# Optimization experiments

Measured on AMD Instinct MI355X. Metric: run time of the kernel, lower is better.

The kernel has to match this reference:

```python
import jax, jax.numpy as jnp
import numpy as np

# Config (matches init_kwargs + Mamba2 defaults: expand=2, headdim=64, ngroups=1)
B_, C_IN, T, H, W = 4, 23, 8, 128, 128
P = 4
DM = 256
D_STATE = 16
D_CONV = 4
EXPAND = 2
D_INNER = EXPAND * DM            # 512
HEADDIM = 64
NHEADS = D_INNER // HEADDIM      # 8
CONV_DIM = D_INNER + 2 * D_STATE # 544 (ngroups=1)
D_IN_PROJ = 2 * D_INNER + 2 * D_STATE + NHEADS


def setup_inputs() -> dict:
    key = jax.random.key(0)
    ks = jax.random.split(key, 12)
    s = lambda k, shape, sc: (jax.random.normal(k, shape, jnp.float32) * sc)
    x = jax.random.normal(ks[0], (B_, C_IN, T, H, W), jnp.float32)
    patch_w = s(ks[1], (DM, C_IN, P, P), 0.05)       # Conv3d weight, depth-1 dim squeezed
    patch_b = s(ks[2], (DM,), 0.02)
    W_in = s(ks[3], (DM, D_IN_PROJ), 0.05)           # in_proj (bias=False)
    conv_w = s(ks[4], (CONV_DIM, D_CONV), 0.2)       # depthwise conv1d weight
    conv_b = s(ks[5], (CONV_DIM,), 0.02)
    dt_bias = jnp.log(jnp.expm1(jnp.exp(jax.random.uniform(ks[6], (NHEADS,), jnp.float32, jnp.log(1e-3), jnp.log(1e-1)))))
    A_log = jnp.log(jnp.arange(1, NHEADS + 1, dtype=jnp.float32))
    D_param = jnp.ones((NHEADS,), jnp.float32)
    norm_w = jnp.ones((D_INNER,), jnp.float32)
    W_out = s(ks[7], (D_INNER, DM), 0.05)            # out_proj (bias=False)
    unembed_w = s(ks[8], (DM, C_IN, P, P), 0.05)     # ConvTranspose3d weight (in,out,1,p,p)
    unembed_b = s(ks[9], (C_IN,), 0.02)
    return {"x": x, "patch_w": patch_w, "patch_b": patch_b, "W_in": W_in,
            "conv_w": conv_w, "conv_b": conv_b, "dt_bias": dt_bias, "A_log": A_log,
            "D_param": D_param, "norm_w": norm_w, "W_out": W_out,
            "unembed_w": unembed_w, "unembed_b": unembed_b}


def reference(x, patch_w, patch_b, W_in, conv_w, conv_b, dt_bias, A_log,
              D_param, norm_w, W_out, unembed_w, unembed_b):
    B, C, Tt, Hh, Ww = x.shape
    p = patch_w.shape[-1]
    Hp, Wp = Hh // p, Ww // p
    L = Tt * Hp * Wp
    # --- Conv3d patch embed (kernel (1,p,p), stride (1,p,p)) == non-overlapping patchify ---
    xr = x.reshape(B, C, Tt, Hp, p, Wp, p)
    emb = jnp.einsum('bcthiwj,dcij->bthwd', xr, patch_w) + patch_b  # [B,T,Hp,Wp,D]
    xs = emb.reshape(B, L, DM)
    # --- Mamba2 ---
    zxbcdt = xs @ W_in                                 # [B,L,2*d_inner+2*d_state+nheads]
    z = zxbcdt[:, :, :D_INNER]
    xBC = zxbcdt[:, :, D_INNER:D_INNER + CONV_DIM]
    dt = zxbcdt[:, :, D_INNER + CONV_DIM:]             # [B,L,nheads]
    # causal depthwise conv1d + silu
    xp = jnp.pad(xBC, ((0, 0), (D_CONV - 1, 0), (0, 0)))
    conv_out = conv_b + sum(xp[:, k:k + L, :] * conv_w[:, k] for k in range(D_CONV))
    xBC = jax.nn.silu(conv_out)
    xh = xBC[:, :, :D_INNER].reshape(B, L, NHEADS, HEADDIM)
    Bm = xBC[:, :, D_INNER:D_INNER + D_STATE]          # [B,L,N] (ngroups=1)
    Cm = xBC[:, :, D_INNER + D_STATE:]                 # [B,L,N]
    dt = jax.nn.softplus(dt + dt_bias)                 # [B,L,H]
    A = -jnp.exp(A_log)                                # [H]
    dA = jnp.exp(dt * A)                               # [B,L,H]
    xdt = xh * dt[..., None]                           # [B,L,H,P]
    # selective state-space scan: h_t = dA_t h_{t-1} + (dt_t x_t) B_t^T ; y_t = h_t C_t
    def step(h, inp):
        dA_t, xdt_t, B_t, C_t = inp
        h = dA_t[..., None, None] * h + jnp.einsum('bhp,bn->bhpn', xdt_t, B_t)
        y = jnp.einsum('bhpn,bn->bhp', h, C_t)
        return h, y
    inps = (dA.transpose(1, 0, 2), xdt.transpose(1, 0, 2, 3),
            Bm.transpose(1, 0, 2), Cm.transpose(1, 0, 2))
    h0 = jnp.zeros((B, NHEADS, HEADDIM, D_STATE), xs.dtype)
    _, ys = jax.lax.scan(step, h0, inps)               # [L,B,H,P]
    y = ys.transpose(1, 0, 2, 3) + D_param[None, None, :, None] * xh
    y = y.reshape(B, L, D_INNER)
    # gated RMSNorm (norm_before_gate=False): rmsnorm(y * silu(z)) * w
    yg = y * jax.nn.silu(z)
    y = yg * jax.lax.rsqrt(jnp.mean(yg * yg, axis=-1, keepdims=True) + 1e-5) * norm_w
    out_seq = y @ W_out                                # [B,L,DM]
    # --- ConvTranspose3d unembed (kernel (1,p,p), stride (1,p,p)) == un-patchify ---
    outp = out_seq.reshape(B, Tt, Hp, Wp, DM)
    un = jnp.einsum('bthwd,dcij->bcthiwj', outp, unembed_w)
    out = un.reshape(B, C, Tt, Hh, Ww) + unembed_b[None, :, None, None, None]
    return out + x
```

## Files before the change

### kernel.cpp

```cpp
#include <hip/hip_runtime.h>
#include <hip/hip_bf16.h>
#include <cstdint>
#include <cstddef>

#define B_N       4
#define C_INCH    23
#define T_N       8
#define W_IMG     128
#define L_SEQ     8192
#define BLROWS    32768
#define DM_       256
#define D_INNER_  512
#define CONV_DIM_ 544
#define D_PROJ    1064
#define KPATCH    368
#define QCH       64
#define NCH       128
#define RECW      56

typedef unsigned short ushort_t;
typedef unsigned int uint_t;
typedef __attribute__((ext_vector_type(8))) short short8;
typedef __attribute__((ext_vector_type(4))) float f32x4;

__device__ __forceinline__ float b2f(ushort_t u) {
    union { float f; uint_t u; } v; v.u = ((uint_t)u) << 16; return v.f;
}
__device__ __forceinline__ ushort_t f2b(float f) {
    union { float f; uint_t u; } v; v.f = f;
    uint_t r = v.u + 0x7fffu + ((v.u >> 16) & 1u);
    return (ushort_t)(r >> 16);
}

__device__ __forceinline__ void gload_lds16(const ushort_t* g, ushort_t* l) {
    __builtin_amdgcn_global_load_lds(
        (const __attribute__((address_space(1))) unsigned int*)g,
        (__attribute__((address_space(3))) unsigned int*)l, 16, 0, 0);
}

__device__ __forceinline__ short8 frag8(const float* q, bool live) {
    short8 f;
    if (live) {
        float4 lo = *(const float4*)q, hi = *(const float4*)(q + 4);
        f[0] = (short)f2b(lo.x); f[1] = (short)f2b(lo.y);
        f[2] = (short)f2b(lo.z); f[3] = (short)f2b(lo.w);
        f[4] = (short)f2b(hi.x); f[5] = (short)f2b(hi.y);
        f[6] = (short)f2b(hi.z); f[7] = (short)f2b(hi.w);
    } else {
        #pragma unroll
        for (int e = 0; e < 8; ++e) f[e] = 0;
    }
    return f;
}

__device__ __forceinline__ uint_t gate2(uint_t yw, uint_t zw) {
    float y0 = b2f((ushort_t)(yw & 0xffffu)), y1 = b2f((ushort_t)(yw >> 16));
    float z0 = b2f((ushort_t)(zw & 0xffffu)), z1 = b2f((ushort_t)(zw >> 16));
    return (uint_t)f2b(y0 * z0) | ((uint_t)f2b(y1 * z1) << 16);
}

__global__ void k_transcast(const float* __restrict__ src, ushort_t* __restrict__ dst,
                            int K, int N, const float* __restrict__ rscale) {
    int n = blockIdx.x;
    for (int k = threadIdx.x; k < K; k += 256) {
        float v = 0.f;
        if (n < N) {
            v = src[(size_t)k * N + n];
            if (rscale) v *= rscale[k];
        }
        dst[(size_t)n * K + k] = f2b(v);
    }
}

__global__ void k_castpad(const float* __restrict__ src, ushort_t* __restrict__ dst) {
    int d = blockIdx.x; int k = threadIdx.x;
    dst[d * 384 + k] = (k < KPATCH) ? f2b(src[d * KPATCH + k]) : (ushort_t)0;
}

__global__ void __launch_bounds__(256) k_pgemm(const float* __restrict__ x,
                                               const ushort_t* __restrict__ Wt,
                                               ushort_t* __restrict__ Cv,
                                               const float* __restrict__ bias) {
    __shared__ ushort_t Al[128 * 64];
    __shared__ ushort_t Bl[128 * 64];
    const int tid = threadIdx.x;
    const int w = tid >> 6, lane = tid & 63;
    const int wr = w >> 1, wc = w & 1;
    const int rowbase = blockIdx.y * 128;
    const int colbase = blockIdx.x * 128;
    const int g = lane >> 4, r = lane & 15;
    const int b  = rowbase >> 13;
    const int t  = (rowbase >> 10) & 7;
    const int hp0 = (rowbase >> 5) & 31;

    f32x4 acc[4][4];
    #pragma unroll
    for (int i = 0; i < 4; ++i)
        #pragma unroll
        for (int j = 0; j < 4; ++j) acc[i][j] = (f32x4){0.f, 0.f, 0.f, 0.f};

    for (int it = 0; it < 6; ++it) {
        int k0 = it * 64;
        __syncthreads();
        #pragma unroll
        for (int i2 = 0; i2 < 4; ++i2) {
            int s = i2 * 256 + (w << 6) + lane;
            int row = s >> 3;
            int c16 = (s & 7) ^ (row & 7);
            gload_lds16(Wt + (size_t)(colbase + row) * 384 + k0 + c16 * 8,
                        &Bl[(size_t)(i2 * 256 + (w << 6)) * 8]);
        }
        #pragma unroll
        for (int i2 = 0; i2 < 8; ++i2) {
            int idx = i2 * 256 + tid;
            int row = idx >> 4, kq = idx & 15;
            int c = (k0 >> 4) + (kq >> 2);
            int i = kq & 3;
            uint_t u0 = 0, u1 = 0;
            if (c < C_INCH) {
                int hp = hp0 + (row >> 5), wp = row & 31;
                const float4 v = *(const float4*)&x[(((size_t)(b * C_INCH + c) * T_N + t) << 14)
                                                    + (size_t)(hp * 4 + i) * W_IMG + wp * 4];
                u0 = (uint_t)f2b(v.x) | ((uint_t)f2b(v.y) << 16);
                u1 = (uint_t)f2b(v.z) | ((uint_t)f2b(v.w) << 16);
            }
            int slot = (row << 3) + ((kq >> 1) ^ (row & 7));
            *(uint2*)&Al[(size_t)slot * 8 + (kq & 1) * 4] = make_uint2(u0, u1);
        }
        __syncthreads();

        short8 af[2][4], bf[2][4];
        #pragma unroll
        for (int ks = 0; ks < 2; ++ks)
            #pragma unroll
            for (int mi = 0; mi < 4; ++mi) {
                int row = (wr << 6) + (mi << 4) + r;
                int c16 = ((ks << 2) | g) ^ (row & 7);
                af[ks][mi] = *(const short8*)&Al[(size_t)((row << 3) + c16) * 8];
            }
        #pragma unroll
        for (int ks = 0; ks < 2; ++ks)
            #pragma unroll
            for (int ni = 0; ni < 4; ++ni) {
                int row = (wc << 6) + (ni << 4) + r;
                int c16 = ((ks << 2) | g) ^ (row & 7);
                bf[ks][ni] = *(const short8*)&Bl[(size_t)((row << 3) + c16) * 8];
            }
        #pragma unroll
        for (int ks = 0; ks < 2; ++ks)
            #pragma unroll
            for (int mi = 0; mi < 4; ++mi)
                #pragma unroll
                for (int ni = 0; ni < 4; ++ni)
                    acc[mi][ni] = __builtin_amdgcn_mfma_f32_16x16x32_bf16(
                        af[ks][mi], bf[ks][ni], acc[mi][ni], 0, 0, 0);
    }

    #pragma unroll
    for (int mi = 0; mi < 4; ++mi) {
        int rw = rowbase + (wr << 6) + (mi << 4) + (g << 2);
        #pragma unroll
        for (int ni = 0; ni < 4; ++ni) {
            int col = colbase + (wc << 6) + (ni << 4) + r;
            float bv = bias[col];
            f32x4 v = acc[mi][ni];
            #pragma unroll
            for (int j = 0; j < 4; ++j)
                Cv[(size_t)(rw + j) * DM_ + col] = f2b(v[j] + bv);
        }
    }
}

template <int K, int N, bool CBF, bool ASCALE, bool SILU>
__global__ void __launch_bounds__(256) k_mgemm(const ushort_t* __restrict__ A, const int lda,
                                               const ushort_t* __restrict__ Wt,
                                               void* __restrict__ Cv, const int ldc, const int coff,
                                               const float* __restrict__ bias) {
    __shared__ ushort_t Al[128 * 64];
    __shared__ ushort_t Bl[128 * 64];
    const int tid = threadIdx.x;
    const int w = tid >> 6, lane = tid & 63;
    const int wr = w >> 1, wc = w & 1;
    const int rowbase = blockIdx.y * 128;
    const int colbase = blockIdx.x * 128;
    const int g = lane >> 4, r = lane & 15;

    f32x4 acc[4][4];
    #pragma unroll
    for (int i = 0; i < 4; ++i)
        #pragma unroll
        for (int j = 0; j < 4; ++j) acc[i][j] = (f32x4){0.f, 0.f, 0.f, 0.f};
    float rs[4] = {0.f, 0.f, 0.f, 0.f};

    for (int k0 = 0; k0 < K; k0 += 64) {
        __syncthreads();
        #pragma unroll
        for (int it = 0; it < 4; ++it) {
            int s = it * 256 + (w << 6) + lane;
            int row = s >> 3;
            int c16 = (s & 7) ^ (row & 7);
            gload_lds16(A + (size_t)(rowbase + row) * lda + k0 + c16 * 8,
                        &Al[(size_t)(it * 256 + (w << 6)) * 8]);
        }
        #pragma unroll
        for (int it = 0; it < 4; ++it) {
            int s = it * 256 + (w << 6) + lane;
            int row = s >> 3;
            int c16 = (s & 7) ^ (row & 7);
            gload_lds16(Wt + (size_t)(colbase + row) * K + k0 + c16 * 8,
                        &Bl[(size_t)(it * 256 + (w << 6)) * 8]);
        }
        __syncthreads();

        short8 af[2][4], bf[2][4];
        #pragma unroll
        for (int ks = 0; ks < 2; ++ks)
            #pragma unroll
            for (int mi = 0; mi < 4; ++mi) {
                int row = (wr << 6) + (mi << 4) + r;
                int c16 = ((ks << 2) | g) ^ (row & 7);
                af[ks][mi] = *(const short8*)&Al[(size_t)((row << 3) + c16) * 8];
            }
        #pragma unroll
        for (int ks = 0; ks < 2; ++ks)
            #pragma unroll
            for (int ni = 0; ni < 4; ++ni) {
                int row = (wc << 6) + (ni << 4) + r;
                int c16 = ((ks << 2) | g) ^ (row & 7);
                bf[ks][ni] = *(const short8*)&Bl[(size_t)((row << 3) + c16) * 8];
            }
        if (ASCALE) {
            #pragma unroll
            for (int ks = 0; ks < 2; ++ks)
                #pragma unroll
                for (int mi = 0; mi < 4; ++mi)
                    #pragma unroll
                    for (int e = 0; e < 8; ++e) {
                        float v = b2f((ushort_t)af[ks][mi][e]);
                        rs[mi] += v * v;
                    }
        }
        #pragma unroll
        for (int ks = 0; ks < 2; ++ks)
            #pragma unroll
            for (int mi = 0; mi < 4; ++mi)
                #pragma unroll
                for (int ni = 0; ni < 4; ++ni)
                    acc[mi][ni] = __builtin_amdgcn_mfma_f32_16x16x32_bf16(
                        af[ks][mi], bf[ks][ni], acc[mi][ni], 0, 0, 0);
    }

    #pragma unroll
    for (int mi = 0; mi < 4; ++mi) {
        int rw = rowbase + (wr << 6) + (mi << 4) + (g << 2);
        float sj[4] = {1.f, 1.f, 1.f, 1.f};
        if (ASCALE) {
            float s = rs[mi];
            s += __shfl_xor(s, 16);
            s += __shfl_xor(s, 32);
            float sc = rsqrtf(s * (1.f / 512.f) + 1e-5f);
            #pragma unroll
            for (int j = 0; j < 4; ++j) sj[j] = __shfl(sc, 4 * g + j);
        }
        #pragma unroll
        for (int ni = 0; ni < 4; ++ni) {
            int col = colbase + (wc << 6) + (ni << 4) + r;
            if (col < N) {
                float bv = bias ? bias[col] : 0.f;
                f32x4 v = acc[mi][ni];
                #pragma unroll
                for (int j = 0; j < 4; ++j) {
                    size_t cidx = (size_t)(rw + j) * ldc + coff + col;
                    float vr = v[j] * sj[j] + bv;
                    if (SILU) vr = vr / (1.f + __expf(-vr));
                    if (CBF) ((ushort_t*)Cv)[cidx] = f2b(vr);
                    else     ((float*)Cv)[cidx]   = vr;
                }
            }
        }
    }
}

__global__ void __launch_bounds__(256) k_conv(const ushort_t* __restrict__ xbcdt,
                                              const float* __restrict__ cw,
                                              const float* __restrict__ cb,
                                              const float* __restrict__ dtb,
                                              const float* __restrict__ alog,
                                              ushort_t* __restrict__ xbc,
                                              float* __restrict__ brec) {
    int tid = threadIdx.x;
    int rb = blockIdx.x * 8;
    int srb = rb & (L_SEQ - 1);
    #pragma unroll
    for (int it = 0; it < 3; ++it) {
        int ch = it * 256 + tid;
        if (ch >= 552) break;
        if (ch < CONV_DIM_) {
            float w0 = cw[ch * 4 + 0], w1 = cw[ch * 4 + 1];
            float w2 = cw[ch * 4 + 2], w3 = cw[ch * 4 + 3];
            float bias = cb[ch];
            float win[11];
            #pragma unroll
            for (int j = 0; j < 11; ++j) {
                int sj = srb + j - 3;
                win[j] = (sj >= 0) ? b2f(xbcdt[(size_t)(rb + j - 3) * 640 + ch]) : 0.f;
            }
            #pragma unroll
            for (int r = 0; r < 8; ++r) {
                float acc = bias + win[r] * w0 + win[r + 1] * w1 + win[r + 2] * w2 + win[r + 3] * w3;
                float s = acc / (1.f + __expf(-acc));
                size_t row = rb + r;
                if (ch < 512) xbc[row * 512 + ch] = f2b(s);
                else          brec[row * RECW + (ch - 512)] = s;
            }
        } else {
            int h = ch - CONV_DIM_;
            float A = -__expf(alog[h]);
            float db = dtb[h];
            #pragma unroll
            for (int r = 0; r < 8; ++r) {
                size_t row = rb + r;
                float v = b2f(xbcdt[row * 640 + ch]) + db;
                float sp = (v > 20.f) ? v : log1pf(__expf(v));
                brec[row * RECW + 32 + h] = __expf(sp * A);
                brec[row * RECW + 40 + h] = sp;
                brec[row * RECW + 48 + h] = sp * A;
            }
        }
    }
}

__device__ __forceinline__ void stage_xht(const ushort_t* __restrict__ xbc,
                                          size_t row0, int h, int tid,
                                          ushort_t* __restrict__ XhT) {
    int j = tid & 63, q4 = tid >> 6;
    const uint4* xsrc = (const uint4*)(xbc + (row0 + j) * 512 + h * 64);
    uint4 xa = xsrc[q4 * 2], xb = xsrc[q4 * 2 + 1];
    #pragma unroll
    for (int pp = 0; pp < 16; ++pp) {
        int p = q4 * 16 + pp;
        uint4 v = (pp < 8) ? xa : xb;
        int sub = (pp >> 1) & 3;
        uint_t word = (sub == 0) ? v.x : (sub == 1) ? v.y : (sub == 2) ? v.z : v.w;
        XhT[p * 72 + j] = (ushort_t)((pp & 1) ? (word >> 16) : (word & 0xffffu));
    }
}

__global__ void __launch_bounds__(256) k_scan1m(const ushort_t* __restrict__ xbc,
                                                const float* __restrict__ brec,
                                                float* __restrict__ sbuf,
                                                float* __restrict__ cdf) {
    __shared__ ushort_t XhT[64 * 72];
    __shared__ float    Bst[64 * 20];
    __shared__ ushort_t BwT[16 * 72];
    const int c = blockIdx.x, h = blockIdx.y, b = blockIdx.z;
    const int tid = threadIdx.x;
    const int w = tid >> 6, lane = tid & 63;
    const int g = lane >> 4, r = lane & 15;
    const size_t row0 = (size_t)b * L_SEQ + (size_t)c * QCH;

    {
        int row = tid >> 2, q = tid & 3;
        float4 v = *(const float4*)(brec + (row0 + row) * RECW + q * 4);
        *(float4*)&Bst[row * 20 + q * 4] = v;
    }
    stage_xht(xbc, row0, h, tid, XhT);

    if (w == 0) {
        float ldA = brec[(row0 + lane) * RECW + 48 + h];
        float dtv = brec[(row0 + lane) * RECW + 40 + h];
        float S = ldA;
        #pragma unroll
        for (int d = 1; d < 64; d <<= 1) {
            float o = __shfl(S, (lane >= d) ? (lane - d) : 0);
            if (lane >= d) S += o;
        }
        float Stot = __shfl(S, 63);
        float wj = dtv * __expf(Stot - S);
        __builtin_amdgcn_s_barrier();
        const float* bp = &Bst[lane * 20];
        float4 b0 = *(const float4*)bp;
        float4 b1 = *(const float4*)(bp + 4);
        float4 b2 = *(const float4*)(bp + 8);
        float4 b3 = *(const float4*)(bp + 12);
        float bv[16] = {b0.x,b0.y,b0.z,b0.w, b1.x,b1.y,b1.z,b1.w,
                        b2.x,b2.y,b2.z,b2.w, b3.x,b3.y,b3.z,b3.w};
        #pragma unroll
        for (int n = 0; n < 16; ++n)
            BwT[n * 72 + lane] = f2b(bv[n] * wj);
        if (lane == 63) cdf[(b * 8 + h) * NCH + c] = __expf(S);
    } else {
        __builtin_amdgcn_s_barrier();
    }
    __syncthreads();

    short8 bwtf[2];
    bwtf[0] = *(const short8*)&BwT[r * 72 + 0  + g * 8];
    bwtf[1] = *(const short8*)&BwT[r * 72 + 32 + g * 8];

    size_t base = ((size_t)(b * 8 + h) * NCH + c) * 1024;
    {
        int p0t = w;
        short8 a0 = *(const short8*)&XhT[(p0t * 16 + r) * 72 + 0  + g * 8];
        short8 a1 = *(const short8*)&XhT[(p0t * 16 + r) * 72 + 32 + g * 8];
        f32x4 acc = (f32x4){0.f, 0.f, 0.f, 0.f};
        acc = __builtin_amdgcn_mfma_f32_16x16x32_bf16(a0, bwtf[0], acc, 0, 0, 0);
        acc = __builtin_amdgcn_mfma_f32_16x16x32_bf16(a1, bwtf[1], acc, 0, 0, 0);
        #pragma unroll
        for (int reg = 0; reg < 4; ++reg)
            sbuf[base + (size_t)(p0t * 16 + g * 4 + reg) * 16 + r] = acc[reg];
    }
}

__global__ void __launch_bounds__(256) k_chain(const float* __restrict__ sbuf,
                                               const float* __restrict__ cdf,
                                               float* __restrict__ hin) {
    int h = blockIdx.x, b = blockIdx.y;
    int tid = threadIdx.x;
    float4 H = make_float4(0.f, 0.f, 0.f, 0.f);
    size_t base = (size_t)((b * 8 + h) * NCH) * 1024;
    for (int c = 0; c < NCH; ++c) {
        *(float4*)&hin[base + (size_t)c * 1024 + tid * 4] = H;
        float cdfv = cdf[(b * 8 + h) * NCH + c];
        float4 S = *(const float4*)&sbuf[base + (size_t)c * 1024 + tid * 4];
        H.x = cdfv * H.x + S.x;
        H.y = cdfv * H.y + S.y;
        H.z = cdfv * H.z + S.z;
        H.w = cdfv * H.w + S.w;
    }
}

__global__ void __launch_bounds__(256) k_ssc2(const ushort_t* __restrict__ xbc,
                                              const ushort_t* __restrict__ z_bf,
                                              const float* __restrict__ brec,
                                              const float* __restrict__ Dp,
                                              const float* __restrict__ hin,
                                              ushort_t* __restrict__ yg_out) {
    __shared__ ushort_t XhT[64 * 72];
    __shared__ ushort_t Pl [64 * 72];
    __shared__ float Sl[64], Tl[64], El[64];
    const int c = blockIdx.x, h = blockIdx.y, b = blockIdx.z;
    const int tid = threadIdx.x;
    const int w = tid >> 6, lane = tid & 63;
    const int g = lane >> 4, r = lane & 15;
    const size_t row0 = (size_t)b * L_SEQ + (size_t)c * QCH;
    const size_t bhc = (size_t)(b * 8 + h) * NCH + c;

    #pragma unroll
    for (int it2 = 0; it2 < 2; ++it2) {
        int idx = it2 * 256 + tid;
        int row = idx >> 3, q = idx & 7;
        float4 v = *(const float4*)(brec + (row0 + row) * RECW + q * 4);
        uint_t u0 = (uint_t)f2b(v.x) | ((uint_t)f2b(v.y) << 16);
        uint_t u1 = (uint_t)f2b(v.z) | ((uint_t)f2b(v.w) << 16);
        *(uint2*)&Pl[row * 40 + q * 4] = make_uint2(u0, u1);
    }
    stage_xht(xbc, row0, h, tid, XhT);

    if (w == 0) {
        float ldA = brec[(row0 + lane) * RECW + 48 + h];
        float dtv = brec[(row0 + lane) * RECW + 40 + h];
        float S = ldA;
        #pragma unroll
        for (int d = 1; d < 64; d <<= 1) {
            float o = __shfl(S, (lane >= d) ? (lane - d) : 0);
            if (lane >= d) S += o;
        }
        Sl[lane] = S;
        Tl[lane] = S - __logf(dtv);
        El[lane] = __expf(S);
    }
    __syncthreads();

    short8 cwf, bwf[4];
    #pragma unroll
    for (int t4 = 0; t4 < 4; ++t4) {
        if (g < 2) {
            bwf[t4] = *(const short8*)&Pl[(t4 * 16 + r) * 40 + 0 + g * 8];
        } else {
            #pragma unroll
            for (int e = 0; e < 8; ++e) bwf[t4][e] = 0;
        }
    }
    if (g < 2) {
        cwf = *(const short8*)&Pl[(w * 16 + r) * 40 + 16 + g * 8];
    } else {
        #pragma unroll
        for (int e = 0; e < 8; ++e) cwf[e] = 0;
    }
    __syncthreads();

    {
        int i = w * 16 + r;
        float si = Sl[i];
        #pragma unroll
        for (int j0t = 0; j0t < 4; ++j0t) {
            f32x4 m = (f32x4){0.f, 0.f, 0.f, 0.f};
            m = __builtin_amdgcn_mfma_f32_16x16x32_bf16(bwf[j0t], cwf, m, 0, 0, 0);
            float4 tj = *(const float4*)&Tl[j0t * 16 + g * 4];
            ushort_t pv[4];
            #pragma unroll
            for (int reg = 0; reg < 4; ++reg) {
                int j = j0t * 16 + g * 4 + reg;
                float tjv = (reg == 0) ? tj.x : (reg == 1) ? tj.y : (reg == 2) ? tj.z : tj.w;
                float mask = (j <= i) ? __expf(si - tjv) : 0.f;
                pv[reg] = f2b(m[reg] * mask);
            }
            uint2 packed = make_uint2((uint_t)pv[0] | ((uint_t)pv[1] << 16),
                                      (uint_t)pv[2] | ((uint_t)pv[3] << 16));
            *(uint2*)&Pl[i * 72 + j0t * 16 + g * 4] = packed;
        }
    }
    __syncthreads();

    short8 pa0 = *(const short8*)&Pl[(w * 16 + r) * 72 + 0  + g * 8];
    short8 pa1 = *(const short8*)&Pl[(w * 16 + r) * 72 + 32 + g * 8];
    short8 xhf[4][2];
    #pragma unroll
    for (int p0t = 0; p0t < 4; ++p0t)
        #pragma unroll
        for (int kk = 0; kk < 2; ++kk)
            xhf[p0t][kk] = *(const short8*)&XhT[(p0t * 16 + r) * 72 + kk * 32 + g * 8];
    short8 hinf[4];
    #pragma unroll
    for (int p0t = 0; p0t < 4; ++p0t)
        hinf[p0t] = frag8(hin + bhc * 1024 + (size_t)(p0t * 16 + r) * 16 + g * 8, g < 2);

    const float Dh = Dp[h];
    float4 e4 = *(const float4*)&El[w * 16 + g * 4];
    __syncthreads();

    #pragma unroll
    for (int p0t = 0; p0t < 4; ++p0t) {
        f32x4 acc = (f32x4){0.f, 0.f, 0.f, 0.f};
        acc = __builtin_amdgcn_mfma_f32_16x16x32_bf16(cwf, hinf[p0t], acc, 0, 0, 0);
        acc[0] *= e4.x; acc[1] *= e4.y; acc[2] *= e4.z; acc[3] *= e4.w;
        acc = __builtin_amdgcn_mfma_f32_16x16x32_bf16(pa0, xhf[p0t][0], acc, 0, 0, 0);
        acc = __builtin_amdgcn_mfma_f32_16x16x32_bf16(pa1, xhf[p0t][1], acc, 0, 0, 0);
        int p = p0t * 16 + r;
        #pragma unroll
        for (int reg = 0; reg < 4; ++reg) {
            int i = w * 16 + g * 4 + reg;
            float xhv = b2f(XhT[p * 72 + i]);
            Pl[i * 72 + p] = f2b(acc[reg] + Dh * xhv);
        }
    }
    __syncthreads();

    #pragma unroll
    for (int it6 = 0; it6 < 2; ++it6) {
        int t = it6 * 256 + tid;
        int i = t >> 3, seg = t & 7;
        size_t row = row0 + i;
        uint4 yv = *(const uint4*)&Pl[i * 72 + seg * 8];
        uint4 zv = *(const uint4*)(z_bf + row * 512 + h * 64 + seg * 8);
        uint4 ov;
        ov.x = gate2(yv.x, zv.x);
        ov.y = gate2(yv.y, zv.y);
        ov.z = gate2(yv.z, zv.z);
        ov.w = gate2(yv.w, zv.w);
        *(uint4*)(yg_out + row * 512 + h * 64 + seg * 8) = ov;
    }
}

__global__ void __launch_bounds__(256) k_scatter(const ushort_t* __restrict__ tmp,
                                                 const float* __restrict__ ub,
                                                 const float* __restrict__ xin,
                                                 float* __restrict__ out) {
    int tid = threadIdx.x;
    int w = tid & 127;
    int h = (blockIdx.x << 1) | (tid >> 7);
    int c = blockIdx.y >> 3, t = blockIdx.y & 7;
    int b = blockIdx.z;
    size_t row = (size_t)b * L_SEQ + t * 1024 + (h >> 2) * 32 + (w >> 2);
    int kk = c * 16 + (h & 3) * 4 + (w & 3);
    size_t oidx = (((size_t)(b * C_INCH + c) * T_N + t) << 14) + (size_t)h * W_IMG + w;
    out[oidx] = b2f(tmp[row * KPATCH + kk]) + ub[c] + xin[oidx];
}

extern "C" void kernel_launch(void* const* d_in, const int* in_sizes, int n_in,
                              void* d_out, int out_size, void* d_ws, size_t ws_size,
                              hipStream_t stream) {
    const float* x       = (const float*)d_in[0];
    const float* patch_w = (const float*)d_in[1];
    const float* patch_b = (const float*)d_in[2];
    const float* W_in    = (const float*)d_in[3];
    const float* conv_w  = (const float*)d_in[4];
    const float* conv_b  = (const float*)d_in[5];
    const float* dt_bias = (const float*)d_in[6];
    const float* A_log   = (const float*)d_in[7];
    const float* D_param = (const float*)d_in[8];
    const float* norm_w  = (const float*)d_in[9];
    const float* W_out   = (const float*)d_in[10];
    const float* unemb_w = (const float*)d_in[11];
    const float* unemb_b = (const float*)d_in[12];
    float* out = (float*)d_out;

    char* p = (char*)d_ws;
    ushort_t* scratch = (ushort_t*)p; p += (size_t)BLROWS * 384 * 2;
    float* cdf  = (float*)p;   p += (size_t)32 * NCH * 4;
    float* sbuf = (float*)p;   p += (size_t)32 * NCH * 1024 * 4;
    float* hin  = (float*)p;   p += (size_t)32 * NCH * 1024 * 4;
    float* brec = (float*)p;   p += (size_t)BLROWS * RECW * 4;
    ushort_t* Wt_p   = (ushort_t*)p; p += (size_t)256 * 384 * 2;
    ushort_t* Wt_in  = (ushort_t*)p; p += (size_t)1152 * 256 * 2;
    ushort_t* Wt_out = (ushort_t*)p; p += (size_t)256 * 512 * 2;
    ushort_t* Wt_un  = (ushort_t*)p; p += (size_t)384 * 256 * 2;
    ushort_t* xs     = (ushort_t*)p; p += (size_t)BLROWS * DM_ * 2;
    ushort_t* xbc    = (ushort_t*)p; p += (size_t)BLROWS * 512 * 2;
    ushort_t* z_bf   = (ushort_t*)p; p += (size_t)BLROWS * 512 * 2;
    ushort_t* xbcdt  = (ushort_t*)p; p += (size_t)BLROWS * 640 * 2;
    size_t need = (size_t)(p - (char*)d_ws);
    if (ws_size < need) return;

    ushort_t* tmp = scratch;
    ushort_t* yg  = xbcdt;

    k_castpad<<<256, 384, 0, stream>>>(patch_w, Wt_p);
    k_transcast<<<1152, 256, 0, stream>>>(W_in, Wt_in, 256, 1064, nullptr);
    k_transcast<<<256, 256, 0, stream>>>(W_out, Wt_out, 512, 256, norm_w);
    k_transcast<<<384, 256, 0, stream>>>(unemb_w, Wt_un, 256, 368, nullptr);

    k_pgemm<<<dim3(2, 256), 256, 0, stream>>>(x, Wt_p, xs, patch_b);

    k_mgemm<256, 512, true, false, true><<<dim3(4, 256), 256, 0, stream>>>(xs, 256, Wt_in, z_bf, 512, 0, nullptr);
    k_mgemm<256, 552, true, false, false><<<dim3(5, 256), 256, 0, stream>>>(xs, 256, Wt_in + (size_t)512 * 256, xbcdt, 640, 0, nullptr);

    k_conv<<<BLROWS / 8, 256, 0, stream>>>(xbcdt, conv_w, conv_b, dt_bias, A_log, xbc, brec);

    k_scan1m<<<dim3(NCH, 8, 4), 256, 0, stream>>>(xbc, brec, sbuf, cdf);
    k_chain<<<dim3(8, 4), 256, 0, stream>>>(sbuf, cdf, hin);
    k_ssc2<<<dim3(NCH, 8, 4), 256, 0, stream>>>(xbc, z_bf, brec, D_param, hin, yg);

    k_mgemm<512, 256, true, true, false><<<dim3(2, 256), 256, 0, stream>>>(yg, 512, Wt_out, xs, DM_, 0, nullptr);

    k_mgemm<256, 368, true, false, false><<<dim3(3, 256), 256, 0, stream>>>(xs, 256, Wt_un, tmp, KPATCH, 0, nullptr);

    k_scatter<<<dim3(64, 184, 4), 256, 0, stream>>>(tmp, unemb_b, x, out);
}
```

Baseline: 243.4 us.

## Fold out_proj and unembed weights into one combined GEMM; unroll chain loop

```diff
diff --git a/kernel.cpp b/kernel.cpp
--- a/kernel.cpp
+++ b/kernel.cpp
@@ -60,14 +60,10 @@
 }
 
 __global__ void k_transcast(const float* __restrict__ src, ushort_t* __restrict__ dst,
-                            int K, int N, const float* __restrict__ rscale) {
+                            int K, int N) {
     int n = blockIdx.x;
     for (int k = threadIdx.x; k < K; k += 256) {
-        float v = 0.f;
-        if (n < N) {
-            v = src[(size_t)k * N + n];
-            if (rscale) v *= rscale[k];
-        }
+        float v = (n < N) ? src[(size_t)k * N + n] : 0.f;
         dst[(size_t)n * K + k] = f2b(v);
     }
 }
@@ -75,6 +71,33 @@
 __global__ void k_castpad(const float* __restrict__ src, ushort_t* __restrict__ dst) {
     int d = blockIdx.x; int k = threadIdx.x;
     dst[d * 384 + k] = (k < KPATCH) ? f2b(src[d * KPATCH + k]) : (ushort_t)0;
+}
+
+__global__ void __launch_bounds__(256) k_wcomb(const float* __restrict__ W_out,
+                                               const float* __restrict__ W_un,
+                                               const float* __restrict__ nw,
+                                               ushort_t* __restrict__ Wt) {
+    int n = blockIdx.x;
+    int tid = threadIdx.x;
+    #pragma unroll
+    for (int half = 0; half < 2; ++half) {
+        int mp = half * 256 + tid;
+        float acc = 0.f;
+        if (n < KPATCH) {
+            const float4* wo4 = (const float4*)(W_out + (size_t)mp * 256);
+            #pragma unroll 4
+            for (int d4 = 0; d4 < 64; ++d4) {
+                float4 wo = wo4[d4];
+                int d = d4 * 4;
+                acc += wo.x * W_un[(size_t)(d + 0) * KPATCH + n]
+                     + wo.y * W_un[(size_t)(d + 1) * KPATCH + n]
+                     + wo.z * W_un[(size_t)(d + 2) * KPATCH + n]
+                     + wo.w * W_un[(size_t)(d + 3) * KPATCH + n];
+            }
+            acc *= nw[mp];
+        }
+        Wt[(size_t)n * 512 + mp] = f2b(acc);
+    }
 }
 
 __global__ void __launch_bounds__(256) k_pgemm(const float* __restrict__ x,
@@ -419,14 +442,23 @@
     int tid = threadIdx.x;
     float4 H = make_float4(0.f, 0.f, 0.f, 0.f);
     size_t base = (size_t)((b * 8 + h) * NCH) * 1024;
-    for (int c = 0; c < NCH; ++c) {
-        *(float4*)&hin[base + (size_t)c * 1024 + tid * 4] = H;
-        float cdfv = cdf[(b * 8 + h) * NCH + c];
-        float4 S = *(const float4*)&sbuf[base + (size_t)c * 1024 + tid * 4];
-        H.x = cdfv * H.x + S.x;
-        H.y = cdfv * H.y + S.y;
-        H.z = cdfv * H.z + S.z;
-        H.w = cdfv * H.w + S.w;
+    const float* cdp = cdf + (size_t)(b * 8 + h) * NCH;
+    for (int c0 = 0; c0 < NCH; c0 += 4) {
+        float4 S[4];
+        float cd[4];
+        #pragma unroll
+        for (int j = 0; j < 4; ++j) {
+            S[j]  = *(const float4*)&sbuf[base + (size_t)(c0 + j) * 1024 + tid * 4];
+            cd[j] = cdp[c0 + j];
+        }
+        #pragma unroll
+        for (int j = 0; j < 4; ++j) {
+            *(float4*)&hin[base + (size_t)(c0 + j) * 1024 + tid * 4] = H;
+            H.x = cd[j] * H.x + S[j].x;
+            H.y = cd[j] * H.y + S[j].y;
+            H.z = cd[j] * H.z + S[j].z;
+            H.w = cd[j] * H.w + S[j].w;
+        }
     }
 }
 
@@ -602,10 +634,9 @@
     float* sbuf = (float*)p;   p += (size_t)32 * NCH * 1024 * 4;
     float* hin  = (float*)p;   p += (size_t)32 * NCH * 1024 * 4;
     float* brec = (float*)p;   p += (size_t)BLROWS * RECW * 4;
-    ushort_t* Wt_p   = (ushort_t*)p; p += (size_t)256 * 384 * 2;
-    ushort_t* Wt_in  = (ushort_t*)p; p += (size_t)1152 * 256 * 2;
-    ushort_t* Wt_out = (ushort_t*)p; p += (size_t)256 * 512 * 2;
-    ushort_t* Wt_un  = (ushort_t*)p; p += (size_t)384 * 256 * 2;
+    ushort_t* Wt_p    = (ushort_t*)p; p += (size_t)256 * 384 * 2;
+    ushort_t* Wt_in   = (ushort_t*)p; p += (size_t)1152 * 256 * 2;
+    ushort_t* Wt_comb = (ushort_t*)p; p += (size_t)384 * 512 * 2;
     ushort_t* xs     = (ushort_t*)p; p += (size_t)BLROWS * DM_ * 2;
     ushort_t* xbc    = (ushort_t*)p; p += (size_t)BLROWS * 512 * 2;
     ushort_t* z_bf   = (ushort_t*)p; p += (size_t)BLROWS * 512 * 2;
@@ -617,9 +648,8 @@
     ushort_t* yg  = xbcdt;
 
     k_castpad<<<256, 384, 0, stream>>>(patch_w, Wt_p);
-    k_transcast<<<1152, 256, 0, stream>>>(W_in, Wt_in, 256, 1064, nullptr);
-    k_transcast<<<256, 256, 0, stream>>>(W_out, Wt_out, 512, 256, norm_w);
-    k_transcast<<<384, 256, 0, stream>>>(unemb_w, Wt_un, 256, 368, nullptr);
+    k_transcast<<<1152, 256, 0, stream>>>(W_in, Wt_in, 256, 1064);
+    k_wcomb<<<384, 256, 0, stream>>>(W_out, unemb_w, norm_w, Wt_comb);
 
     k_pgemm<<<dim3(2, 256), 256, 0, stream>>>(x, Wt_p, xs, patch_b);
 
@@ -632,9 +662,7 @@
     k_chain<<<dim3(8, 4), 256, 0, stream>>>(sbuf, cdf, hin);
     k_ssc2<<<dim3(NCH, 8, 4), 256, 0, stream>>>(xbc, z_bf, brec, D_param, hin, yg);
 
-    k_mgemm<512, 256, true, true, false><<<dim3(2, 256), 256, 0, stream>>>(yg, 512, Wt_out, xs, DM_, 0, nullptr);
-
-    k_mgemm<256, 368, true, false, false><<<dim3(3, 256), 256, 0, stream>>>(xs, 256, Wt_un, tmp, KPATCH, 0, nullptr);
+    k_mgemm<512, 368, true, true, false><<<dim3(3, 256), 256, 0, stream>>>(yg, 512, Wt_comb, tmp, KPATCH, 0, nullptr);
 
     k_scatter<<<dim3(64, 184, 4), 256, 0, stream>>>(tmp, unemb_b, x, out);
 }
```

Measured after the change: 285.1 us. 17.1% more time.
